# Performance work log

Hardware: AMD Instinct MI355X
Metric: run time of the kernel (lower is better)

## Reference

```python
import jax, jax.numpy as jnp
import numpy as np

KS = (7, 7)
ST = (3, 3)
PD = (3, 3)
DIM = 512
HID = 1960  # 40 * 49, divisible by kernel_shape


def _patch_flat_idx(out_h, out_w):
    kh, kw = KS; sh, sw = ST; ph, pw = PD
    oh = (out_h + 2 * ph - kh) // sh + 1
    ow = (out_w + 2 * pw - kw) // sw + 1
    Wp = out_w + 2 * pw
    iy = jnp.arange(kh)[:, None, None, None] + (jnp.arange(oh) * sh)[None, None, :, None]
    ix = jnp.arange(kw)[None, :, None, None] + (jnp.arange(ow) * sw)[None, None, None, :]
    # (kh, kw, oh, ow) flat index into padded image
    return (iy * Wp + ix), oh, ow


def fold(patches, out_h, out_w):
    # patches: (B, C*kh*kw, L) -> (B, C, out_h, out_w), overlap-add like F.fold
    kh, kw = KS; ph, pw = PD
    idx, oh, ow = _patch_flat_idx(out_h, out_w)
    B, CK, L = patches.shape
    C = CK // (kh * kw)
    Hp, Wp = out_h + 2 * ph, out_w + 2 * pw
    p = patches.reshape(B, C, kh, kw, oh, ow)
    out = jnp.zeros((B, C, Hp * Wp), patches.dtype)
    out = out.at[:, :, idx.reshape(-1)].add(p.reshape(B, C, -1))
    return out.reshape(B, C, Hp, Wp)[:, :, ph:ph + out_h, pw:pw + out_w]


def unfold(img, out_h, out_w):
    # img: (B, C, H, W) -> (B, C*kh*kw, L), like F.unfold
    kh, kw = KS; ph, pw = PD
    idx, oh, ow = _patch_flat_idx(out_h, out_w)
    B, C = img.shape[:2]
    imgp = jnp.pad(img, ((0, 0), (0, 0), (ph, ph), (pw, pw)))
    flat = imgp.reshape(B, C, -1)
    g = flat[:, :, idx.reshape(-1)].reshape(B, C, kh, kw, oh, ow)
    return g.reshape(B, C * kh * kw, oh * ow)


def setup_inputs() -> dict:
    key = jax.random.key(0)
    k1, k2, k3, k4, k5 = jax.random.split(key, 5)
    x = jax.random.normal(k1, (2, 5760, DIM), dtype=jnp.float32)
    W1 = jax.random.normal(k2, (HID, DIM), dtype=jnp.float32) * 0.02
    b1 = jax.random.normal(k3, (HID,), dtype=jnp.float32) * 0.02
    W2 = jax.random.normal(k4, (DIM, HID), dtype=jnp.float32) * 0.02
    b2 = jax.random.normal(k5, (DIM,), dtype=jnp.float32) * 0.02
    return {"x": x, "W1": W1, "b1": b1, "W2": W2, "b2": b2, "out_h": 60, "out_w": 108}


def reference(x, W1, b1, W2, b2, out_h, out_w):
    kh, kw = KS; sh, sw = ST; ph, pw = PD
    oh = (out_h + 2 * ph - kh) // sh + 1
    ow = (out_w + 2 * pw - kw) // sw + 1
    n_vecs = oh * ow
    h = jnp.einsum('bnd,hd->bnh', x, W1) + b1          # (b, n, HID)
    b_, n, c = h.shape
    p = h.reshape(-1, n_vecs, c).transpose(0, 2, 1)     # (B', c, L)
    folded = fold(p, out_h, out_w)                      # (B', c//49, H, W)
    ones = jnp.ones((p.shape[0], kh * kw, n_vecs), h.dtype)
    norm = fold(ones, out_h, out_w)                     # (B', 1, H, W)
    y = unfold(folded / norm, out_h, out_w)             # (B', c, L)
    y = y.transpose(0, 2, 1).reshape(b_, n, c)
    out = jnp.einsum('bnh,dh->bnd', jax.nn.gelu(y, approximate=False), W2) + b2
    return out
```

## Files before the change

kernel.cpp:

```cpp
#include <hip/hip_runtime.h>
#include <cmath>

#define M_ROWS   11520
#define DIM      512
#define HID      1960
#define HIDP     2048
#define KP2      1984
#define OH       20
#define OW       36
#define LVEC     720
#define NCH      40
#define BPRIME   16
#define HP       66
#define WP       114

typedef unsigned short u16;
typedef __bf16 bf16x8 __attribute__((ext_vector_type(8)));
typedef float  f32x4  __attribute__((ext_vector_type(4)));

__device__ __forceinline__ u16 f2bf(float f) {
    unsigned u = __float_as_uint(f);
    u += 0x7fffu + ((u >> 16) & 1u);
    return (u16)(u >> 16);
}
__device__ __forceinline__ float bf2f(u16 h) {
    return __uint_as_float(((unsigned)h) << 16);
}

__device__ __forceinline__ void gload_lds16(const void* g, void* l) {
    __builtin_amdgcn_global_load_lds(
        (const __attribute__((address_space(1))) void*)g,
        (__attribute__((address_space(3))) void*)l, 16, 0, 0);
}

#define CVT_XB   5760
#define CVT_W1B  1024
__global__ __launch_bounds__(256) void cvt_all(const float* __restrict__ x,
                                               const float* __restrict__ W1,
                                               const float* __restrict__ W2,
                                               u16* __restrict__ xb,
                                               u16* __restrict__ W1b,
                                               u16* __restrict__ W2b) {
    const int b = blockIdx.x;
    const int tid = threadIdx.x;
    ushort4 o;
    if (b < CVT_XB) {
        int i = (b * 256 + tid) * 4;
        float4 v = *(const float4*)(x + i);
        o.x = f2bf(v.x); o.y = f2bf(v.y); o.z = f2bf(v.z); o.w = f2bf(v.w);
        *(ushort4*)(xb + i) = o;
    } else if (b < CVT_XB + CVT_W1B) {
        int i = ((b - CVT_XB) * 256 + tid) * 4;
        if (i < HID * DIM) {
            float4 v = *(const float4*)(W1 + i);
            o.x = f2bf(v.x); o.y = f2bf(v.y); o.z = f2bf(v.z); o.w = f2bf(v.w);
        } else {
            o.x = o.y = o.z = o.w = 0;
        }
        *(ushort4*)(W1b + i) = o;
    } else {
        int i = ((b - CVT_XB - CVT_W1B) * 256 + tid) * 4;
        int d = i / HIDP, c = i - d * HIDP;
        if (c < HID) {
            float4 v = *(const float4*)(W2 + (size_t)d * HID + c);
            o.x = f2bf(v.x); o.y = f2bf(v.y); o.z = f2bf(v.z); o.w = f2bf(v.w);
        } else {
            o.x = o.y = o.z = o.w = 0;
        }
        *(ushort4*)(W2b + i) = o;
    }
}

template <int OUT_BF16, int BN>
__global__ __launch_bounds__(512) void gemm_bt(const u16* __restrict__ A,
                                               const u16* __restrict__ B,
                                               const float* __restrict__ bias,
                                               int biasN, void* __restrict__ Cout,
                                               int N, int K, int ldk) {
    constexpr int WN = BN / 2;
    constexpr int NU = WN / 16;
    constexpr int BCH = BN * 8;

    __shared__ u16 sA[128 * 64];
    __shared__ u16 sB[BN * 64];

    const int tid  = threadIdx.x;
    const int ntn  = N / BN;
    const int NB   = gridDim.x;
    const int v    = (blockIdx.x & 7) * (NB >> 3) + (blockIdx.x >> 3);
    const int bm   = v / ntn;
    const int bn   = v - bm * ntn;
    const int lane = tid & 63;
    const int wv   = tid >> 6;
    const int wm   = (wv >> 1) * 32;
    const int wn   = (wv & 1) * WN;
    const int r    = lane & 15;
    const int quad = lane >> 4;

    const size_t Arow0 = (size_t)bm * 128 * ldk;
    const size_t Brow0 = (size_t)bn * BN * ldk;

    f32x4 acc[2][NU] = {};

    for (int kt = 0; kt < K; kt += 64) {
        __syncthreads();
#pragma unroll
        for (int i = 0; i < 2; i++) {
            int e   = i * 512 + tid;
            int row = e >> 3;
            int cp  = e & 7;
            int cg  = cp ^ (row & 7);
            gload_lds16(A + Arow0 + (size_t)row * ldk + kt + cg * 8, (char*)sA + e * 16);
        }
#pragma unroll
        for (int i = 0; i < BCH / 512; i++) {
            int e   = i * 512 + tid;
            int row = e >> 3;
            int cp  = e & 7;
            int cg  = cp ^ (row & 7);
            gload_lds16(B + Brow0 + (size_t)row * ldk + kt + cg * 8, (char*)sB + e * 16);
        }
        __syncthreads();
#pragma unroll
        for (int kk = 0; kk < 2; kk++) {
            bf16x8 af[2], bg[NU];
#pragma unroll
            for (int t = 0; t < 2; t++) {
                int row = wm + t * 16 + r;
                int c   = (kk * 4 + quad) ^ (row & 7);
                af[t] = *(const bf16x8*)(sA + row * 64 + c * 8);
            }
#pragma unroll
            for (int u = 0; u < NU; u++) {
                int row = wn + u * 16 + r;
                int c   = (kk * 4 + quad) ^ (row & 7);
                bg[u] = *(const bf16x8*)(sB + row * 64 + c * 8);
            }
#pragma unroll
            for (int t = 0; t < 2; t++)
#pragma unroll
                for (int u = 0; u < NU; u++)
                    acc[t][u] = __builtin_amdgcn_mfma_f32_16x16x32_bf16(
                        af[t], bg[u], acc[t][u], 0, 0, 0);
        }
    }

    const int gm0 = bm * 128 + wm;
    const int gn0 = bn * BN + wn;
#pragma unroll
    for (int u = 0; u < NU; u++) {
        int gn = gn0 + u * 16 + r;
        float bv = (gn < biasN) ? bias[gn] : 0.0f;
#pragma unroll
        for (int t = 0; t < 2; t++) {
            int gm = gm0 + t * 16 + quad * 4;
#pragma unroll
            for (int q = 0; q < 4; q++) {
                float v2 = acc[t][u][q] + bv;
                if (OUT_BF16)
                    ((u16*)Cout)[(size_t)(gm + q) * N + gn] = f2bf(v2);
                else
                    ((float*)Cout)[(size_t)(gm + q) * N + gn] = v2;
            }
        }
    }
}

__global__ __launch_bounds__(256) void midA_fold(const u16* __restrict__ hg,
                                                 u16* __restrict__ G) {
    __shared__ u16 sh[7 * OW * 49];

    const int b  = blockIdx.x;
    const int bp = b / (NCH * 4);
    const int rr = b - bp * (NCH * 4);
    const int ch = rr >> 2;
    const int s  = rr & 3;
    const int lo    = (s == 0) ? 0 : (5 * s - 2);
    const int nload = (s == 0) ? 5 : 7;
    const int row0  = 15 * s;
    const int nrows = (s == 3) ? 21 : 15;
    const int n0 = bp * LVEC;
    const int c0 = ch * 49;
    const int tid = threadIdx.x;

    for (int i = tid; i < nload * OW * 49; i += 256) {
        int l = i / 49, k = i - l * 49;
        sh[i] = hg[(size_t)(n0 + lo * OW + l) * HIDP + c0 + k];
    }
    __syncthreads();

    const int px = tid & 127;
    const int rg = tid >> 7;
    if (px >= WP) return;

    const bool pxin = (px >= 3) && (px <= 110);
    const int kx0 = px % 3;
    int  ct[3];
    bool vx[3];
    int  cx = 0;
#pragma unroll
    for (int dx = 0; dx < 3; dx++) {
        int kx = kx0 + 3 * dx, rx = px - kx;
        bool ok = pxin && (kx <= 6) && (rx >= 0) && (rx <= 105);
        vx[dx] = ok;
        ct[dx] = ok ? ((rx / 3) * 49 + kx) : 0;
        cx += ok ? 1 : 0;
    }
    const float fcx = (cx == 3) ? (1.0f / 3.0f) : ((cx == 2) ? 0.5f : 1.0f);

    u16* Gb = G + (size_t)(bp * NCH + ch) * (HP * WP);
    for (int ri = rg; ri < nrows; ri += 2) {
        int py = row0 + ri;
        float val = 0.0f;
        if (pxin && py >= 3 && py <= 62) {
            int ky0 = py % 3;
            float sum = 0.0f;
            int cy = 0;
#pragma unroll
            for (int dy = 0; dy < 3; dy++) {
                int ky = ky0 + 3 * dy, ry = py - ky;
                if (ky <= 6 && ry >= 0 && ry <= 57) {
                    int rt = (ry / 3 - lo) * (OW * 49) + ky * 7;
                    cy++;
                    float v0 = bf2f(sh[rt + ct[0]]);
                    float v1 = bf2f(sh[rt + ct[1]]);
                    float v2 = bf2f(sh[rt + ct[2]]);
                    sum += vx[0] ? v0 : 0.0f;
                    sum += vx[1] ? v1 : 0.0f;
                    sum += vx[2] ? v2 : 0.0f;
                }
            }
            float fcy = (cy == 3) ? (1.0f / 3.0f) : ((cy == 2) ? 0.5f : 1.0f);
            float m = sum * fcx * fcy;
            val = 0.5f * m * (1.0f + erff(m * 0.70710678118654752f));
        }
        Gb[py * WP + px] = f2bf(val);
    }
}

__global__ __launch_bounds__(256) void midB_unfold(const u16* __restrict__ G,
                                                   u16* __restrict__ hg) {
    __shared__ u16 sG[34 * WP];

    const int b  = blockIdx.x;
    const int bp = b / (NCH * 2);
    const int rr = b - bp * (NCH * 2);
    const int ch = rr >> 1;
    const int s  = rr & 1;
    const int o0 = s * 10;
    const int n0 = bp * LVEC + o0 * OW;
    const int c0 = ch * 49;
    const int tid = threadIdx.x;

    const u16* Gb = G + (size_t)(bp * NCH + ch) * (HP * WP) + 3 * o0 * WP;
    for (int p = tid; p < 34 * WP; p += 256) sG[p] = Gb[p];
    __syncthreads();

    for (int i = tid; i < 10 * OW * 49; i += 256) {
        int l = i / 49, k = i - l * 49;
        int ky = k / 7, kx = k - ky * 7;
        int oy = l / OW, ox = l - oy * OW;
        hg[(size_t)(n0 + l) * HIDP + c0 + k] = sG[(3 * oy + ky) * WP + kx + 3 * ox];
    }
}

extern "C" void kernel_launch(void* const* d_in, const int* in_sizes, int n_in,
                              void* d_out, int out_size, void* d_ws, size_t ws_size,
                              hipStream_t stream) {
    (void)in_sizes; (void)n_in; (void)out_size; (void)ws_size;
    const float* x  = (const float*)d_in[0];
    const float* W1 = (const float*)d_in[1];
    const float* b1 = (const float*)d_in[2];
    const float* W2 = (const float*)d_in[3];
    const float* b2 = (const float*)d_in[4];
    float* out = (float*)d_out;

    char* ws = (char*)d_ws;
    u16* xb  = (u16*)(ws);
    u16* W1b = (u16*)(ws + 11796480);
    u16* W2b = (u16*)(ws + 11796480 + 2097152);
    u16* hg  = (u16*)(ws + 11796480 + 2097152 + 2097152);
    u16* G   = xb;

    cvt_all<<<CVT_XB + 2 * CVT_W1B, 256, 0, stream>>>(x, W1, W2, xb, W1b, W2b);

    gemm_bt<1, 128><<<(M_ROWS / 128) * (HIDP / 128), 512, 0, stream>>>(
        xb, W1b, b1, HID, (void*)hg, HIDP, DIM, DIM);

    midA_fold<<<BPRIME * NCH * 4, 256, 0, stream>>>(hg, G);
    midB_unfold<<<BPRIME * NCH * 2, 256, 0, stream>>>(G, hg);

    gemm_bt<0, 64><<<(M_ROWS / 128) * (DIM / 64), 512, 0, stream>>>(
        hg, W2b, b2, DIM, (void*)out, DIM, KP2, HIDP);
}
```

Measured before the change: 204.3 us.

## Fuse fold+GELU and unfold into one kernel via shared memory

Merges the fold/normalize/GELU kernel and the unfold kernel into a single kernel. Each block loads 12 patch rows into LDS, computes its 34-row folded image slab into LDS, and unfolds it straight into a new buffer g2. This removes the round trip of the intermediate image G through global memory and one kernel launch. In exchange, overlapping patch rows are loaded redundantly by the two halves, LDS use per block rises, and the padding columns of g2 are now zeroed inside the conversion kernel.

```diff
diff --git a/kernel.cpp b/kernel.cpp
--- a/kernel.cpp
+++ b/kernel.cpp
@@ -35,12 +35,15 @@
 
 #define CVT_XB   5760
 #define CVT_W1B  1024
+#define CVT_W2B  1024
+#define CVT_Z    270
 __global__ __launch_bounds__(256) void cvt_all(const float* __restrict__ x,
                                                const float* __restrict__ W1,
                                                const float* __restrict__ W2,
                                                u16* __restrict__ xb,
                                                u16* __restrict__ W1b,
-                                               u16* __restrict__ W2b) {
+                                               u16* __restrict__ W2b,
+                                               u16* __restrict__ g2) {
     const int b = blockIdx.x;
     const int tid = threadIdx.x;
     ushort4 o;
@@ -58,7 +61,7 @@
             o.x = o.y = o.z = o.w = 0;
         }
         *(ushort4*)(W1b + i) = o;
-    } else {
+    } else if (b < CVT_XB + CVT_W1B + CVT_W2B) {
         int i = ((b - CVT_XB - CVT_W1B) * 256 + tid) * 4;
         int d = i / HIDP, c = i - d * HIDP;
         if (c < HID) {
@@ -68,6 +71,11 @@
             o.x = o.y = o.z = o.w = 0;
         }
         *(ushort4*)(W2b + i) = o;
+    } else {
+        int i = ((b - CVT_XB - CVT_W1B - CVT_W2B) * 256 + tid) * 4;
+        int row = i / 24, c = i - row * 24;
+        o.x = o.y = o.z = o.w = 0;
+        *(ushort4*)(g2 + (size_t)row * HIDP + HID + c) = o;
     }
 }
 
@@ -166,80 +174,9 @@
     }
 }
 
-__global__ __launch_bounds__(256) void midA_fold(const u16* __restrict__ hg,
-                                                 u16* __restrict__ G) {
-    __shared__ u16 sh[7 * OW * 49];
-
-    const int b  = blockIdx.x;
-    const int bp = b / (NCH * 4);
-    const int rr = b - bp * (NCH * 4);
-    const int ch = rr >> 2;
-    const int s  = rr & 3;
-    const int lo    = (s == 0) ? 0 : (5 * s - 2);
-    const int nload = (s == 0) ? 5 : 7;
-    const int row0  = 15 * s;
-    const int nrows = (s == 3) ? 21 : 15;
-    const int n0 = bp * LVEC;
-    const int c0 = ch * 49;
-    const int tid = threadIdx.x;
-
-    for (int i = tid; i < nload * OW * 49; i += 256) {
-        int l = i / 49, k = i - l * 49;
-        sh[i] = hg[(size_t)(n0 + lo * OW + l) * HIDP + c0 + k];
-    }
-    __syncthreads();
-
-    const int px = tid & 127;
-    const int rg = tid >> 7;
-    if (px >= WP) return;
-
-    const bool pxin = (px >= 3) && (px <= 110);
-    const int kx0 = px % 3;
-    int  ct[3];
-    bool vx[3];
-    int  cx = 0;
-#pragma unroll
-    for (int dx = 0; dx < 3; dx++) {
-        int kx = kx0 + 3 * dx, rx = px - kx;
-        bool ok = pxin && (kx <= 6) && (rx >= 0) && (rx <= 105);
-        vx[dx] = ok;
-        ct[dx] = ok ? ((rx / 3) * 49 + kx) : 0;
-        cx += ok ? 1 : 0;
-    }
-    const float fcx = (cx == 3) ? (1.0f / 3.0f) : ((cx == 2) ? 0.5f : 1.0f);
-
-    u16* Gb = G + (size_t)(bp * NCH + ch) * (HP * WP);
-    for (int ri = rg; ri < nrows; ri += 2) {
-        int py = row0 + ri;
-        float val = 0.0f;
-        if (pxin && py >= 3 && py <= 62) {
-            int ky0 = py % 3;
-            float sum = 0.0f;
-            int cy = 0;
-#pragma unroll
-            for (int dy = 0; dy < 3; dy++) {
-                int ky = ky0 + 3 * dy, ry = py - ky;
-                if (ky <= 6 && ry >= 0 && ry <= 57) {
-                    int rt = (ry / 3 - lo) * (OW * 49) + ky * 7;
-                    cy++;
-                    float v0 = bf2f(sh[rt + ct[0]]);
-                    float v1 = bf2f(sh[rt + ct[1]]);
-                    float v2 = bf2f(sh[rt + ct[2]]);
-                    sum += vx[0] ? v0 : 0.0f;
-                    sum += vx[1] ? v1 : 0.0f;
-                    sum += vx[2] ? v2 : 0.0f;
-                }
-            }
-            float fcy = (cy == 3) ? (1.0f / 3.0f) : ((cy == 2) ? 0.5f : 1.0f);
-            float m = sum * fcx * fcy;
-            val = 0.5f * m * (1.0f + erff(m * 0.70710678118654752f));
-        }
-        Gb[py * WP + px] = f2bf(val);
-    }
-}
-
-__global__ __launch_bounds__(256) void midB_unfold(const u16* __restrict__ G,
-                                                   u16* __restrict__ hg) {
+__global__ __launch_bounds__(512) void mid_fused(const u16* __restrict__ hg,
+                                                 u16* __restrict__ g2) {
+    __shared__ u16 sh[12 * OW * 49];
     __shared__ u16 sG[34 * WP];
 
     const int b  = blockIdx.x;
@@ -248,19 +185,71 @@
     const int ch = rr >> 1;
     const int s  = rr & 1;
     const int o0 = s * 10;
-    const int n0 = bp * LVEC + o0 * OW;
+    const int lo = s * 8;
+    const int n0 = bp * LVEC;
     const int c0 = ch * 49;
     const int tid = threadIdx.x;
 
-    const u16* Gb = G + (size_t)(bp * NCH + ch) * (HP * WP) + 3 * o0 * WP;
-    for (int p = tid; p < 34 * WP; p += 256) sG[p] = Gb[p];
+    for (int i = tid; i < 12 * OW * 49; i += 512) {
+        int l = i / 49, k = i - l * 49;
+        sh[i] = hg[(size_t)(n0 + lo * OW + l) * HIDP + c0 + k];
+    }
     __syncthreads();
 
-    for (int i = tid; i < 10 * OW * 49; i += 256) {
+    const int px = tid & 127;
+    const int rg = tid >> 7;
+    if (px < WP) {
+        const bool pxin = (px >= 3) && (px <= 110);
+        const int kx0 = px % 3;
+        int  ct[3];
+        bool vx[3];
+        int  cx = 0;
+#pragma unroll
+        for (int dx = 0; dx < 3; dx++) {
+            int kx = kx0 + 3 * dx, rx = px - kx;
+            bool ok = pxin && (kx <= 6) && (rx >= 0) && (rx <= 105);
+            vx[dx] = ok;
+            ct[dx] = ok ? ((rx / 3) * 49 + kx) : 0;
+            cx += ok ? 1 : 0;
+        }
+        const float fcx = (cx == 3) ? (1.0f / 3.0f) : ((cx == 2) ? 0.5f : 1.0f);
+
+        for (int pr = rg; pr < 34; pr += 4) {
+            int py = 3 * o0 + pr;
+            float val = 0.0f;
+            if (pxin && py >= 3 && py <= 62) {
+                int ky0 = py % 3;
+                float sum = 0.0f;
+                int cy = 0;
+#pragma unroll
+                for (int dy = 0; dy < 3; dy++) {
+                    int ky = ky0 + 3 * dy, ry = py - ky;
+                    if (ky <= 6 && ry >= 0 && ry <= 57) {
+                        int rt = (ry / 3 - lo) * (OW * 49) + ky * 7;
+                        cy++;
+                        float v0 = bf2f(sh[rt + ct[0]]);
+                        float v1 = bf2f(sh[rt + ct[1]]);
+                        float v2 = bf2f(sh[rt + ct[2]]);
+                        sum += vx[0] ? v0 : 0.0f;
+                        sum += vx[1] ? v1 : 0.0f;
+                        sum += vx[2] ? v2 : 0.0f;
+                    }
+                }
+                float fcy = (cy == 3) ? (1.0f / 3.0f) : ((cy == 2) ? 0.5f : 1.0f);
+                float m = sum * fcx * fcy;
+                val = 0.5f * m * (1.0f + erff(m * 0.70710678118654752f));
+            }
+            sG[pr * WP + px] = f2bf(val);
+        }
+    }
+    __syncthreads();
+
+    const int nb = (n0 + o0 * OW);
+    for (int i = tid; i < 10 * OW * 49; i += 512) {
         int l = i / 49, k = i - l * 49;
         int ky = k / 7, kx = k - ky * 7;
         int oy = l / OW, ox = l - oy * OW;
-        hg[(size_t)(n0 + l) * HIDP + c0 + k] = sG[(3 * oy + ky) * WP + kx + 3 * ox];
+        g2[(size_t)(nb + l) * HIDP + c0 + k] = sG[(3 * oy + ky) * WP + kx + 3 * ox];
     }
 }
 
@@ -278,18 +267,18 @@
     char* ws = (char*)d_ws;
     u16* xb  = (u16*)(ws);
     u16* W1b = (u16*)(ws + 11796480);
-    u16* W2b = (u16*)(ws + 11796480 + 2097152);
-    u16* hg  = (u16*)(ws + 11796480 + 2097152 + 2097152);
-    u16* G   = xb;
-
-    cvt_all<<<CVT_XB + 2 * CVT_W1B, 256, 0, stream>>>(x, W1, W2, xb, W1b, W2b);
+    u16* W2b = (u16*)(ws + 13893632);
+    u16* hg  = (u16*)(ws + 15990784);
+    u16* g2  = (u16*)(ws + 63176704);
+
+    cvt_all<<<CVT_XB + CVT_W1B + CVT_W2B + CVT_Z, 256, 0, stream>>>(
+        x, W1, W2, xb, W1b, W2b, g2);
 
     gemm_bt<1, 128><<<(M_ROWS / 128) * (HIDP / 128), 512, 0, stream>>>(
         xb, W1b, b1, HID, (void*)hg, HIDP, DIM, DIM);
 
-    midA_fold<<<BPRIME * NCH * 4, 256, 0, stream>>>(hg, G);
-    midB_unfold<<<BPRIME * NCH * 2, 256, 0, stream>>>(G, hg);
+    mid_fused<<<BPRIME * NCH * 2, 512, 0, stream>>>(hg, g2);
 
     gemm_bt<0, 64><<<(M_ROWS / 128) * (DIM / 64), 512, 0, stream>>>(
-        hg, W2b, b2, DIM, (void*)out, DIM, KP2, HIDP);
-}
+        g2, W2b, b2, DIM, (void*)out, DIM, KP2, HIDP);
+}
```

Measured after the change: 198.1 us. 3.1% less time.
